# Performance work log

Hardware: AMD Instinct MI355X
Metric: run time of the kernel (lower is better)

## Reference

```python
import jax, jax.numpy as jnp
import numpy as np

NUM_HEADS = 8
LATENT_FRAME = 4
D_MODEL = 1024
D_FF = 1024  # dim_feedforward == output_dim in the torch module
N_LAYERS = 6
IN_DIM = 128
LN_EPS = 1e-5


def get_slopes(n):
    # standard ALiBi slopes for power-of-two head counts: 2^{-8(i+1)/n}
    return jnp.asarray([2.0 ** (-8.0 * (i + 1) / n) for i in range(n)], jnp.float32)


def alibi_mask(num_heads, T):
    # non-causal ('future') ALiBi: additive bias -slope_h * |i - j|, shape (H, T, T)
    dist = jnp.abs(jnp.arange(T)[:, None] - jnp.arange(T)[None, :]).astype(jnp.float32)
    return -get_slopes(num_heads)[:, None, None] * dist


def layernorm(x, g, b):
    m = jnp.mean(x, axis=-1, keepdims=True)
    v = jnp.mean((x - m) ** 2, axis=-1, keepdims=True)
    return (x - m) * jax.lax.rsqrt(v + LN_EPS) * g + b


def encoder_layer(x, p, mask):
    # torch TransformerEncoderLayer, post-norm, gelu(exact), dropout=0
    B, T, D = x.shape
    H, Dh = NUM_HEADS, D // NUM_HEADS
    qkv = x @ p['in_w'].T + p['in_b']                      # (B,T,3D)
    q, k, v = jnp.split(qkv, 3, axis=-1)
    hsplit = lambda t: t.reshape(B, T, H, Dh).transpose(0, 2, 1, 3)  # (B,H,T,Dh)
    q, k, v = hsplit(q), hsplit(k), hsplit(v)
    scores = jnp.einsum('bhqd,bhkd->bhqk', q, k) / float(np.sqrt(Dh)) + mask[None]
    attn = jax.nn.softmax(scores, axis=-1)
    o = jnp.einsum('bhqk,bhkd->bhqd', attn, v).transpose(0, 2, 1, 3).reshape(B, T, D)
    o = o @ p['out_w'].T + p['out_b']
    x = layernorm(x + o, p['ln1_g'], p['ln1_b'])
    ff = jax.nn.gelu(x @ p['ff1_w'].T + p['ff1_b'], approximate=False) @ p['ff2_w'].T + p['ff2_b']
    return layernorm(x + ff, p['ln2_g'], p['ln2_b'])


def setup_inputs() -> dict:
    key = jax.random.key(0)
    ks = iter(jax.random.split(key, 32))
    s = 0.02
    B, T, F = 8, 2048, IN_DIM
    Fs = F * LATENT_FRAME  # 512
    inp = {
        'x': jax.random.normal(next(ks), (B, T, F), jnp.float32),
        'pre_w': jax.random.normal(next(ks), (D_MODEL, Fs), jnp.float32) * s,
        'pre_b': jnp.zeros((D_MODEL,), jnp.float32),
        'in_w': jax.random.normal(next(ks), (N_LAYERS, 3 * D_MODEL, D_MODEL), jnp.float32) * s,
        'in_b': jnp.zeros((N_LAYERS, 3 * D_MODEL), jnp.float32),
        'out_w': jax.random.normal(next(ks), (N_LAYERS, D_MODEL, D_MODEL), jnp.float32) * s,
        'out_b': jnp.zeros((N_LAYERS, D_MODEL), jnp.float32),
        'ln1_g': jnp.ones((N_LAYERS, D_MODEL), jnp.float32),
        'ln1_b': jnp.zeros((N_LAYERS, D_MODEL), jnp.float32),
        'ff1_w': jax.random.normal(next(ks), (N_LAYERS, D_FF, D_MODEL), jnp.float32) * s,
        'ff1_b': jnp.zeros((N_LAYERS, D_FF), jnp.float32),
        'ff2_w': jax.random.normal(next(ks), (N_LAYERS, D_MODEL, D_FF), jnp.float32) * s,
        'ff2_b': jnp.zeros((N_LAYERS, D_MODEL), jnp.float32),
        'ln2_g': jnp.ones((N_LAYERS, D_MODEL), jnp.float32),
        'ln2_b': jnp.zeros((N_LAYERS, D_MODEL), jnp.float32),
        'post_w': jax.random.normal(next(ks), (D_MODEL, D_MODEL), jnp.float32) * s,
        'post_b': jnp.zeros((D_MODEL,), jnp.float32),
    }
    return inp


def reference(x, pre_w, pre_b, in_w, in_b, out_w, out_b, ln1_g, ln1_b,
              ff1_w, ff1_b, ff2_w, ff2_b, ln2_g, ln2_b, post_w, post_b):
    B, T, F = x.shape
    Tl = T // LATENT_FRAME
    x = x.reshape(B, Tl, F * LATENT_FRAME)
    x = x @ pre_w.T + pre_b                     # (B, Tl, D)
    mask = alibi_mask(NUM_HEADS, Tl)            # (H, Tl, Tl), shared by all batches
    layers = dict(in_w=in_w, in_b=in_b, out_w=out_w, out_b=out_b,
                  ln1_g=ln1_g, ln1_b=ln1_b, ff1_w=ff1_w, ff1_b=ff1_b,
                  ff2_w=ff2_w, ff2_b=ff2_b, ln2_g=ln2_g, ln2_b=ln2_b)
    def step(h, p):
        return encoder_layer(h, p, mask), None
    x, _ = jax.lax.scan(step, x, layers)
    return x @ post_w.T + post_b
```

## Files before the change

kernel.cpp:

```cpp
#include <hip/hip_runtime.h>
#include <hip/hip_bf16.h>

#define B 8
#define TL 512
#define M_ROWS 4096
#define D 1024
#define DFF 1024
#define H 8
#define DH 128
#define NL 6

typedef unsigned short ushort_t;
typedef unsigned int uint_t;
typedef short bf16x8 __attribute__((ext_vector_type(8)));
typedef float f32x4 __attribute__((ext_vector_type(4)));

__device__ __forceinline__ ushort_t f2bf(float f) {
    uint_t u = __float_as_uint(f);
    u += 0x7FFFu + ((u >> 16) & 1u);
    return (ushort_t)(u >> 16);
}
__device__ __forceinline__ float gelu_exact(float x) {
    return 0.5f * x * (1.0f + erff(x * 0.70710678118654752f));
}
__device__ __forceinline__ void gload_lds16(const ushort_t* g, ushort_t* l) {
    __builtin_amdgcn_global_load_lds(
        (const __attribute__((address_space(1))) void*)g,
        (__attribute__((address_space(3))) void*)l, 16, 0, 0);
}

struct CvtArgs {
    const float* s[7];
    ushort_t* d[7];
    int nq[7];
    int bstart[8];
};

__global__ __launch_bounds__(256) void cvt_all(CvtArgs a) {
    const int bid = blockIdx.x;
#pragma unroll
    for (int seg = 0; seg < 7; ++seg) {
        const int b0 = a.bstart[seg], b1 = a.bstart[seg + 1];
        if (bid < b0 || bid >= b1) continue;
        const int stride = (b1 - b0) * 256;
        const float* s = a.s[seg];
        ushort_t* d = a.d[seg];
        const int nq = a.nq[seg];
        for (int i = (bid - b0) * 256 + threadIdx.x; i < nq; i += stride) {
            float4 v = *(const float4*)(s + (size_t)i * 4);
            ushort4 o;
            o.x = f2bf(v.x); o.y = f2bf(v.y); o.z = f2bf(v.z); o.w = f2bf(v.w);
            *(ushort4*)(d + (size_t)i * 4) = o;
        }
    }
}

#define LSLOT64(r, c) (((r) * 8 + ((c) ^ ((r) & 7))) * 8)

#define PIPE_K_LOOP(NT)                                                        \
    {                                                                          \
        stage(0, 0);                                                           \
        stage(1, 64);                                                          \
        int bsel = 0;                                                          \
        for (int t = 0; t < (NT)-1; ++t) {                                     \
            asm volatile("s_waitcnt vmcnt(4)" ::: "memory");                   \
            __builtin_amdgcn_s_barrier();                                      \
            comp(bsel);                                                        \
            if (t + 2 < (NT)) {                                                \
                int nb = bsel + 2; if (nb >= 3) nb -= 3;                       \
                stage(nb, (t + 2) * 64);                                       \
            }                                                                  \
            ++bsel; if (bsel == 3) bsel = 0;                                   \
        }                                                                      \
        asm volatile("s_waitcnt vmcnt(0)" ::: "memory");                       \
        __builtin_amdgcn_s_barrier();                                          \
        comp(bsel);                                                            \
    }

__global__ __launch_bounds__(512) void gemm_n128(
    const ushort_t* __restrict__ A, const ushort_t* __restrict__ W,
    const float* __restrict__ bias, float* __restrict__ Cf,
    ushort_t* __restrict__ Cb, int M, int N, int K, int do_gelu) {
    extern __shared__ ushort_t lds[];

    const int tid = threadIdx.x;
    const int lane = tid & 63;
    const int w = tid >> 6;
    const int wm = w >> 2;
    const int wn = w & 3;
    const int bm = blockIdx.y * 128;
    const int bn = blockIdx.x * 128;
    const int fr = lane & 15;
    const int fq = lane >> 4;

    const ushort_t* gA[2];
    const ushort_t* gB[2];
    int sdst[2];
#pragma unroll
    for (int u = 0; u < 2; ++u) {
        int s = tid + u * 512;
        int r = s >> 3, c = (s & 7) ^ (r & 7);
        gA[u] = A + (size_t)(bm + r) * K + c * 8;
        gB[u] = W + (size_t)(bn + r) * K + c * 8;
        sdst[u] = s * 8;
    }

    int aoff[4][2], boff[2][2];
#pragma unroll
    for (int ti = 0; ti < 4; ++ti)
#pragma unroll
        for (int ks = 0; ks < 2; ++ks)
            aoff[ti][ks] = LSLOT64(wm * 64 + ti * 16 + fr, ks * 4 + fq);
#pragma unroll
    for (int tj = 0; tj < 2; ++tj)
#pragma unroll
        for (int ks = 0; ks < 2; ++ks)
            boff[tj][ks] = LSLOT64(wn * 32 + tj * 16 + fr, ks * 4 + fq);

    f32x4 acc[4][2];
#pragma unroll
    for (int i = 0; i < 4; ++i)
#pragma unroll
        for (int j = 0; j < 2; ++j) acc[i][j] = (f32x4){0.f, 0.f, 0.f, 0.f};

    auto stage = [&](int buf, int k0) {
#pragma unroll
        for (int u = 0; u < 2; ++u)
            gload_lds16(gA[u] + k0, &lds[buf * 16384 + sdst[u]]);
#pragma unroll
        for (int u = 0; u < 2; ++u)
            gload_lds16(gB[u] + k0, &lds[buf * 16384 + 8192 + sdst[u]]);
    };
    auto comp = [&](int buf) {
#pragma unroll
        for (int ks = 0; ks < 2; ++ks) {
            bf16x8 af[4], bfv[2];
#pragma unroll
            for (int ti = 0; ti < 4; ++ti)
                af[ti] = *(const bf16x8*)&lds[buf * 16384 + aoff[ti][ks]];
#pragma unroll
            for (int tj = 0; tj < 2; ++tj)
                bfv[tj] = *(const bf16x8*)&lds[buf * 16384 + 8192 + boff[tj][ks]];
            __builtin_amdgcn_s_setprio(1);
#pragma unroll
            for (int i = 0; i < 4; ++i)
#pragma unroll
                for (int j = 0; j < 2; ++j)
                    acc[i][j] = __builtin_amdgcn_mfma_f32_16x16x32_bf16(
                        af[i], bfv[j], acc[i][j], 0, 0, 0);
            __builtin_amdgcn_s_setprio(0);
        }
    };

    const int NT = K >> 6;
    PIPE_K_LOOP(NT)
    __syncthreads();

    float bv[2];
#pragma unroll
    for (int tj = 0; tj < 2; ++tj) bv[tj] = bias[bn + wn * 32 + tj * 16 + fr];

    float* eps = (float*)lds;
#pragma unroll
    for (int p = 0; p < 2; ++p) {
        if (p) __syncthreads();
        if (wm == p) {
#pragma unroll
            for (int ti = 0; ti < 4; ++ti)
#pragma unroll
                for (int tj = 0; tj < 2; ++tj)
#pragma unroll
                    for (int r = 0; r < 4; ++r) {
                        float v = acc[ti][tj][r] + bv[tj];
                        if (do_gelu) v = gelu_exact(v);
                        eps[(ti * 16 + fq * 4 + r) * 132 +
                            wn * 32 + tj * 16 + fr] = v;
                    }
        }
        __syncthreads();
#pragma unroll
        for (int k = 0; k < 4; ++k) {
            int f = tid + k * 512;
            int row = f >> 5, c4 = f & 31;
            float4 v = *(const float4*)&eps[row * 132 + c4 * 4];
            const size_t off = (size_t)(bm + p * 64 + row) * N + bn + c4 * 4;
            if (Cf) *(float4*)(Cf + off) = v;
            if (Cb) {
                ushort4 ob;
                ob.x = f2bf(v.x); ob.y = f2bf(v.y);
                ob.z = f2bf(v.z); ob.w = f2bf(v.w);
                *(ushort4*)(Cb + off) = ob;
            }
        }
    }
}

__global__ __launch_bounds__(512) void gemm_qkv128(
    const ushort_t* __restrict__ A, const ushort_t* __restrict__ W,
    const float* __restrict__ bias, ushort_t* __restrict__ Qb,
    ushort_t* __restrict__ Kb, ushort_t* __restrict__ Vt) {
    extern __shared__ ushort_t lds[];
    const int K = 1024;

    const int bid = blockIdx.x;
    const int wg = (bid & 7) * 96 + (bid >> 3);
    const int by = wg / 24, bx = wg - by * 24;
    const int bm = by * 128, bn = bx * 128;

    const int tid = threadIdx.x;
    const int lane = tid & 63;
    const int w = tid >> 6;
    const int wm = w >> 2;
    const int wn = w & 3;
    const int fr = lane & 15;
    const int fq = lane >> 4;

    const ushort_t* gA[2];
    const ushort_t* gB[2];
    int sdst[2];
#pragma unroll
    for (int u = 0; u < 2; ++u) {
        int s = tid + u * 512;
        int r = s >> 3, c = (s & 7) ^ (r & 7);
        gA[u] = A + (size_t)(bm + r) * K + c * 8;
        gB[u] = W + (size_t)(bn + r) * K + c * 8;
        sdst[u] = s * 8;
    }

    int aoff[4][2], boff[2][2];
#pragma unroll
    for (int ti = 0; ti < 4; ++ti)
#pragma unroll
        for (int ks = 0; ks < 2; ++ks)
            aoff[ti][ks] = LSLOT64(wm * 64 + ti * 16 + fr, ks * 4 + fq);
#pragma unroll
    for (int tj = 0; tj < 2; ++tj)
#pragma unroll
        for (int ks = 0; ks < 2; ++ks)
            boff[tj][ks] = LSLOT64(wn * 32 + tj * 16 + fr, ks * 4 + fq);

    f32x4 acc[4][2];
#pragma unroll
    for (int i = 0; i < 4; ++i)
#pragma unroll
        for (int j = 0; j < 2; ++j) acc[i][j] = (f32x4){0.f, 0.f, 0.f, 0.f};

    auto stage = [&](int buf, int k0) {
#pragma unroll
        for (int u = 0; u < 2; ++u)
            gload_lds16(gA[u] + k0, &lds[buf * 16384 + sdst[u]]);
#pragma unroll
        for (int u = 0; u < 2; ++u)
            gload_lds16(gB[u] + k0, &lds[buf * 16384 + 8192 + sdst[u]]);
    };
    auto comp = [&](int buf) {
#pragma unroll
        for (int ks = 0; ks < 2; ++ks) {
            bf16x8 af[4], bfv[2];
#pragma unroll
            for (int ti = 0; ti < 4; ++ti)
                af[ti] = *(const bf16x8*)&lds[buf * 16384 + aoff[ti][ks]];
#pragma unroll
            for (int tj = 0; tj < 2; ++tj)
                bfv[tj] = *(const bf16x8*)&lds[buf * 16384 + 8192 + boff[tj][ks]];
            __builtin_amdgcn_s_setprio(1);
#pragma unroll
            for (int i = 0; i < 4; ++i)
#pragma unroll
                for (int j = 0; j < 2; ++j)
                    acc[i][j] = __builtin_amdgcn_mfma_f32_16x16x32_bf16(
                        af[i], bfv[j], acc[i][j], 0, 0, 0);
            __builtin_amdgcn_s_setprio(0);
        }
    };

    PIPE_K_LOOP(16)

    const float qscale = 0.08838834764831845f;
    float bv[2];
#pragma unroll
    for (int tj = 0; tj < 2; ++tj) bv[tj] = bias[bn + wn * 32 + tj * 16 + fr];

    if (bn < 2 * D) {
        __syncthreads();
        const float scale = (bn < D) ? qscale : 1.f;
        ushort_t* dst = (bn < D) ? Qb : Kb;
        const int nc0 = (bn < D) ? bn : bn - D;
        float* eps = (float*)lds;
#pragma unroll
        for (int p = 0; p < 2; ++p) {
            if (p) __syncthreads();
            if (wm == p) {
#pragma unroll
                for (int ti = 0; ti < 4; ++ti)
#pragma unroll
                    for (int tj = 0; tj < 2; ++tj)
#pragma unroll
                        for (int r = 0; r < 4; ++r)
                            eps[(ti * 16 + fq * 4 + r) * 132 +
                                wn * 32 + tj * 16 + fr] =
                                (acc[ti][tj][r] + bv[tj]) * scale;
            }
            __syncthreads();
#pragma unroll
            for (int k = 0; k < 4; ++k) {
                int f = tid + k * 512;
                int row = f >> 5, c4 = f & 31;
                float4 v = *(const float4*)&eps[row * 132 + c4 * 4];
                ushort4 ob;
                ob.x = f2bf(v.x); ob.y = f2bf(v.y);
                ob.z = f2bf(v.z); ob.w = f2bf(v.w);
                *(ushort4*)(dst + (size_t)(bm + p * 64 + row) * D + nc0 +
                            c4 * 4) = ob;
            }
        }
    } else {
#pragma unroll
        for (int tj = 0; tj < 2; ++tj) {
            const int n = bn + wn * 32 + tj * 16 + fr;
            const int h = (n - 2 * D) >> 7;
            const int dh = (n - 2 * D) & 127;
#pragma unroll
            for (int ti = 0; ti < 4; ++ti) {
                const int m0 = bm + wm * 64 + ti * 16 + fq * 4;
                const int bb = m0 >> 9;
                const int t = m0 & 511;
                f32x4 a = acc[ti][tj];
                ushort4 pk;
                pk.x = f2bf(a[0] + bv[tj]); pk.y = f2bf(a[1] + bv[tj]);
                pk.z = f2bf(a[2] + bv[tj]); pk.w = f2bf(a[3] + bv[tj]);
                *(ushort4*)&Vt[((size_t)(bb * H + h) * DH + dh) * TL + t] = pk;
            }
        }
    }
}

#define LSW16(r, g) ((((r) << 4) + ((g) ^ ((r) & 7))) << 3)
#define LSW8(r, g) ((((r) << 3) + ((g) ^ ((r) & 7))) << 3)

__global__ __launch_bounds__(256, 2) void attn_mfma(
    const ushort_t* __restrict__ Qb, const ushort_t* __restrict__ Kb,
    const ushort_t* __restrict__ Vt, ushort_t* __restrict__ Ab) {
    __shared__ ushort_t Qs[64 * 128];
    __shared__ ushort_t Ks[64 * 128];
    __shared__ ushort_t Vts[128 * 64];
    __shared__ ushort_t Ps[64 * 72];

    const int q0 = blockIdx.x * 64;
    const int bh = blockIdx.y;
    const int b = bh >> 3;
    const int h = bh & 7;
    const int tid = threadIdx.x;
    const int lane = tid & 63;
    const int w = tid >> 6;
    const int fr = lane & 15;
    const int fq = lane >> 4;

    const float slope = exp2f(-(float)(h + 1));

#pragma unroll
    for (int kk = 0; kk < 4; ++kk) {
        int s = tid + kk * 256;
        int r = s >> 4, gp = s & 15, gl = gp ^ (r & 7);
        gload_lds16(Qb + (size_t)(b * TL + q0 + r) * D + h * DH + gl * 8,
                    &Qs[s * 8]);
    }

    f32x4 o8[8];
    float m_i[4], l_i[4];
#pragma unroll
    for (int nt = 0; nt < 8; ++nt) o8[nt] = (f32x4){0.f, 0.f, 0.f, 0.f};
#pragma unroll
    for (int r = 0; r < 4; ++r) { m_i[r] = -1e30f; l_i[r] = 0.f; }

    for (int kt = 0; kt < TL / 64; ++kt) {
        __syncthreads();
#pragma unroll
        for (int kk = 0; kk < 4; ++kk) {
            int s = tid + kk * 256;
            int r = s >> 4, gp = s & 15, gl = gp ^ (r & 7);
            gload_lds16(Kb + (size_t)(b * TL + kt * 64 + r) * D + h * DH + gl * 8,
                        &Ks[s * 8]);
        }
#pragma unroll
        for (int kk = 0; kk < 4; ++kk) {
            int s = tid + kk * 256;
            int r = s >> 3, gp = s & 7, gl = gp ^ (r & 7);
            gload_lds16(Vt + ((size_t)bh * DH + r) * TL + kt * 64 + gl * 8,
                        &Vts[s * 8]);
        }
        __syncthreads();

        f32x4 sacc[4];
#pragma unroll
        for (int jt = 0; jt < 4; ++jt) sacc[jt] = (f32x4){0.f, 0.f, 0.f, 0.f};
        __builtin_amdgcn_s_setprio(1);
#pragma unroll
        for (int s4 = 0; s4 < 4; ++s4) {
            bf16x8 aq = *(const bf16x8*)&Qs[LSW16(w * 16 + fr, s4 * 4 + fq)];
#pragma unroll
            for (int jt = 0; jt < 4; ++jt) {
                bf16x8 kb = *(const bf16x8*)&Ks[LSW16(jt * 16 + fr, s4 * 4 + fq)];
                sacc[jt] = __builtin_amdgcn_mfma_f32_16x16x32_bf16(
                    aq, kb, sacc[jt], 0, 0, 0);
            }
        }
        __builtin_amdgcn_s_setprio(0);

        const int iq = q0 + w * 16 + fq * 4;
        const int jk = kt * 64 + fr;
        float al[4];
#pragma unroll
        for (int r = 0; r < 4; ++r) {
            float sv[4];
#pragma unroll
            for (int jt = 0; jt < 4; ++jt)
                sv[jt] = sacc[jt][r] -
                         slope * fabsf((float)(iq + r - jk - jt * 16));
            float mx = fmaxf(fmaxf(sv[0], sv[1]), fmaxf(sv[2], sv[3]));
            mx = fmaxf(mx, __shfl_xor(mx, 1));
            mx = fmaxf(mx, __shfl_xor(mx, 2));
            mx = fmaxf(mx, __shfl_xor(mx, 4));
            mx = fmaxf(mx, __shfl_xor(mx, 8));
            float mnew = fmaxf(m_i[r], mx);
            al[r] = __expf(m_i[r] - mnew);
            float rs = 0.f;
#pragma unroll
            for (int jt = 0; jt < 4; ++jt) {
                sv[jt] = __expf(sv[jt] - mnew);
                rs += sv[jt];
            }
            rs += __shfl_xor(rs, 1);
            rs += __shfl_xor(rs, 2);
            rs += __shfl_xor(rs, 4);
            rs += __shfl_xor(rs, 8);
            l_i[r] = l_i[r] * al[r] + rs;
            m_i[r] = mnew;
            const int prow = w * 16 + fq * 4 + r;
#pragma unroll
            for (int jt = 0; jt < 4; ++jt)
                Ps[prow * 72 + jt * 16 + fr] = f2bf(sv[jt]);
        }
#pragma unroll
        for (int nt = 0; nt < 8; ++nt)
#pragma unroll
            for (int r = 0; r < 4; ++r) o8[nt][r] *= al[r];

        __builtin_amdgcn_s_setprio(1);
#pragma unroll
        for (int s2 = 0; s2 < 2; ++s2) {
            bf16x8 pa = *(const bf16x8*)&Ps[(w * 16 + fr) * 72 + s2 * 32 + fq * 8];
#pragma unroll
            for (int nt = 0; nt < 8; ++nt) {
                bf16x8 vb = *(const bf16x8*)&Vts[LSW8(nt * 16 + fr, s2 * 4 + fq)];
                o8[nt] = __builtin_amdgcn_mfma_f32_16x16x32_bf16(
                    pa, vb, o8[nt], 0, 0, 0);
            }
        }
        __builtin_amdgcn_s_setprio(0);
    }

#pragma unroll
    for (int r = 0; r < 4; ++r) {
        float inv = 1.f / l_i[r];
        const size_t base = (size_t)(b * TL + q0 + w * 16 + fq * 4 + r) * D + h * DH;
#pragma unroll
        for (int nt = 0; nt < 8; ++nt)
            Ab[base + nt * 16 + fr] = f2bf(o8[nt][r] * inv);
    }
}

__global__ __launch_bounds__(256) void add_ln(const float* __restrict__ x,
                                              const float* __restrict__ y,
                                              const float* __restrict__ g,
                                              const float* __restrict__ bta,
                                              float* __restrict__ out,
                                              ushort_t* __restrict__ outb) {
    const int row = blockIdx.x * 4 + (threadIdx.x >> 6);
    const int lane = threadIdx.x & 63;
    const size_t rbase = (size_t)row * D;

    float4 v[4];
#pragma unroll
    for (int j = 0; j < 4; ++j) {
        float4 xv = *(const float4*)(x + rbase + lane * 4 + j * 256);
        float4 yv = *(const float4*)(y + rbase + lane * 4 + j * 256);
        v[j].x = xv.x + yv.x; v[j].y = xv.y + yv.y;
        v[j].z = xv.z + yv.z; v[j].w = xv.w + yv.w;
    }

    float s = 0.f;
#pragma unroll
    for (int j = 0; j < 4; ++j) s += v[j].x + v[j].y + v[j].z + v[j].w;
#pragma unroll
    for (int off = 32; off; off >>= 1) s += __shfl_xor(s, off);
    const float mean = s * (1.f / (float)D);

    float sq = 0.f;
#pragma unroll
    for (int j = 0; j < 4; ++j) {
        float d0 = v[j].x - mean, d1 = v[j].y - mean;
        float d2 = v[j].z - mean, d3 = v[j].w - mean;
        sq += d0 * d0 + d1 * d1 + d2 * d2 + d3 * d3;
    }
#pragma unroll
    for (int off = 32; off; off >>= 1) sq += __shfl_xor(sq, off);
    const float var = sq * (1.f / (float)D);
    const float inv = rsqrtf(var + 1e-5f);

#pragma unroll
    for (int j = 0; j < 4; ++j) {
        const int col = lane * 4 + j * 256;
        float4 gv = *(const float4*)(g + col);
        float4 bv = *(const float4*)(bta + col);
        float4 o;
        o.x = (v[j].x - mean) * inv * gv.x + bv.x;
        o.y = (v[j].y - mean) * inv * gv.y + bv.y;
        o.z = (v[j].z - mean) * inv * gv.z + bv.z;
        o.w = (v[j].w - mean) * inv * gv.w + bv.w;
        *(float4*)(out + rbase + col) = o;
        ushort4 ob;
        ob.x = f2bf(o.x); ob.y = f2bf(o.y); ob.z = f2bf(o.z); ob.w = f2bf(o.w);
        *(ushort4*)(outb + rbase + col) = ob;
    }
}

extern "C" void kernel_launch(void* const* d_in, const int* in_sizes, int n_in,
                              void* d_out, int out_size, void* d_ws, size_t ws_size,
                              hipStream_t stream) {
    const float* x_in   = (const float*)d_in[0];
    const float* pre_w  = (const float*)d_in[1];
    const float* pre_b  = (const float*)d_in[2];
    const float* in_w   = (const float*)d_in[3];
    const float* in_b   = (const float*)d_in[4];
    const float* out_w  = (const float*)d_in[5];
    const float* out_b  = (const float*)d_in[6];
    const float* ln1_g  = (const float*)d_in[7];
    const float* ln1_b  = (const float*)d_in[8];
    const float* ff1_w  = (const float*)d_in[9];
    const float* ff1_b  = (const float*)d_in[10];
    const float* ff2_w  = (const float*)d_in[11];
    const float* ff2_b  = (const float*)d_in[12];
    const float* ln2_g  = (const float*)d_in[13];
    const float* ln2_b  = (const float*)d_in[14];
    const float* post_w = (const float*)d_in[15];
    const float* post_b = (const float*)d_in[16];

    static bool attr_set = false;
    if (!attr_set) {
        hipFuncSetAttribute((const void*)gemm_n128,
                            hipFuncAttributeMaxDynamicSharedMemorySize, 98304);
        hipFuncSetAttribute((const void*)gemm_qkv128,
                            hipFuncAttributeMaxDynamicSharedMemorySize, 98304);
        attr_set = true;
    }

    float* X = (float*)d_ws;
    float* Y = X + (size_t)M_ROWS * D;
    ushort_t* Xb   = (ushort_t*)(Y + (size_t)M_ROWS * D);
    ushort_t* Ab   = Xb + (size_t)M_ROWS * D;
    ushort_t* Qb   = Ab + (size_t)M_ROWS * D;
    ushort_t* Kb   = Qb + (size_t)M_ROWS * D;
    ushort_t* Vt   = Kb + (size_t)M_ROWS * D;
    ushort_t* xinb = Vt + (size_t)M_ROWS * D;
    ushort_t* pwb  = xinb + (size_t)M_ROWS * 512;
    ushort_t* iwb  = pwb + (size_t)D * 512;
    ushort_t* owb  = iwb + (size_t)NL * 3 * D * D;
    ushort_t* f1wb = owb + (size_t)NL * D * D;
    ushort_t* f2wb = f1wb + (size_t)NL * DFF * D;
    ushort_t* powb = f2wb + (size_t)NL * D * DFF;

    const dim3 blk(256);

    CvtArgs ca;
    ca.s[0] = x_in;   ca.d[0] = xinb; ca.nq[0] = (M_ROWS * 512) / 4;
    ca.s[1] = pre_w;  ca.d[1] = pwb;  ca.nq[1] = (D * 512) / 4;
    ca.s[2] = in_w;   ca.d[2] = iwb;  ca.nq[2] = (NL * 3 * D * D) / 4;
    ca.s[3] = out_w;  ca.d[3] = owb;  ca.nq[3] = (NL * D * D) / 4;
    ca.s[4] = ff1_w;  ca.d[4] = f1wb; ca.nq[4] = (NL * DFF * D) / 4;
    ca.s[5] = ff2_w;  ca.d[5] = f2wb; ca.nq[5] = (NL * D * DFF) / 4;
    ca.s[6] = post_w; ca.d[6] = powb; ca.nq[6] = (D * D) / 4;
    {
        long long total = 0;
        for (int i = 0; i < 7; ++i) total += ca.nq[i];
        long long cum = 0;
        ca.bstart[0] = 0;
        for (int i = 0; i < 7; ++i) {
            cum += ca.nq[i];
            ca.bstart[i + 1] = (int)((cum * 4096) / total);
        }
        ca.bstart[7] = 4096;
    }
    cvt_all<<<4096, blk, 0, stream>>>(ca);

    const dim3 gN128(D / 128, M_ROWS / 128);

    gemm_n128<<<gN128, dim3(512), 98304, stream>>>(xinb, pwb, pre_b, X, Xb,
                                                   M_ROWS, D, 512, 0);

    for (int l = 0; l < NL; ++l) {
        gemm_qkv128<<<dim3(768), dim3(512), 98304, stream>>>(
            Xb, iwb + (size_t)l * 3 * D * D, in_b + (size_t)l * 3 * D,
            Qb, Kb, Vt);
        attn_mfma<<<dim3(TL / 64, B * H), blk, 0, stream>>>(Qb, Kb, Vt, Ab);
        gemm_n128<<<gN128, dim3(512), 98304, stream>>>(
            Ab, owb + (size_t)l * D * D, out_b + (size_t)l * D, Y, nullptr,
            M_ROWS, D, D, 0);
        add_ln<<<dim3(M_ROWS / 4), blk, 0, stream>>>(X, Y, ln1_g + (size_t)l * D,
                                                     ln1_b + (size_t)l * D, X, Xb);
        gemm_n128<<<gN128, dim3(512), 98304, stream>>>(
            Xb, f1wb + (size_t)l * DFF * D, ff1_b + (size_t)l * DFF, nullptr, Ab,
            M_ROWS, DFF, D, 1);
        gemm_n128<<<gN128, dim3(512), 98304, stream>>>(
            Ab, f2wb + (size_t)l * D * DFF, ff2_b + (size_t)l * D, Y, nullptr,
            M_ROWS, D, DFF, 0);
        add_ln<<<dim3(M_ROWS / 4), blk, 0, stream>>>(X, Y, ln2_g + (size_t)l * D,
                                                     ln2_b + (size_t)l * D, X, Xb);
    }

    gemm_n128<<<gN128, dim3(512), 98304, stream>>>(Xb, powb, post_b,
                                                   (float*)d_out, nullptr,
                                                   M_ROWS, D, D, 0);
}
```

Before: 1.082 ms.

## Double-buffer GEMM LDS, prefetch K/V in attention, nontemporal weight conversion

The GEMM kernels change from a triple-buffered LDS pipeline to a double-buffered one with an extra barrier per k-step. This cuts dynamic LDS from 96KB to 64KB, which may allow more blocks per CU. The attention kernel holds Q in registers and double-buffers K and V tiles with explicit vmcnt waits, so loads overlap compute instead of being synchronous each iteration. The bf16 conversion kernel uses nontemporal loads and stores. The risk is less latency hiding in the GEMMs and more barrier overhead.

```diff
diff --git a/kernel.cpp b/kernel.cpp
--- a/kernel.cpp
+++ b/kernel.cpp
@@ -12,6 +12,7 @@
 
 typedef unsigned short ushort_t;
 typedef unsigned int uint_t;
+typedef unsigned long long u64_t;
 typedef short bf16x8 __attribute__((ext_vector_type(8)));
 typedef float f32x4 __attribute__((ext_vector_type(4)));
 
@@ -47,34 +48,34 @@
         ushort_t* d = a.d[seg];
         const int nq = a.nq[seg];
         for (int i = (bid - b0) * 256 + threadIdx.x; i < nq; i += stride) {
-            float4 v = *(const float4*)(s + (size_t)i * 4);
-            ushort4 o;
-            o.x = f2bf(v.x); o.y = f2bf(v.y); o.z = f2bf(v.z); o.w = f2bf(v.w);
-            *(ushort4*)(d + (size_t)i * 4) = o;
+            f32x4 v = __builtin_nontemporal_load(
+                (const f32x4*)(s + (size_t)i * 4));
+            u64_t pk = (u64_t)f2bf(v[0]) | ((u64_t)f2bf(v[1]) << 16) |
+                       ((u64_t)f2bf(v[2]) << 32) | ((u64_t)f2bf(v[3]) << 48);
+            __builtin_nontemporal_store(pk, (u64_t*)(d + (size_t)i * 4));
         }
     }
 }
 
 #define LSLOT64(r, c) (((r) * 8 + ((c) ^ ((r) & 7))) * 8)
 
-#define PIPE_K_LOOP(NT)                                                        \
+#define PIPE2_K_LOOP(NT)                                                       \
     {                                                                          \
         stage(0, 0);                                                           \
         stage(1, 64);                                                          \
-        int bsel = 0;                                                          \
         for (int t = 0; t < (NT)-1; ++t) {                                     \
             asm volatile("s_waitcnt vmcnt(4)" ::: "memory");                   \
             __builtin_amdgcn_s_barrier();                                      \
-            comp(bsel);                                                        \
-            if (t + 2 < (NT)) {                                                \
-                int nb = bsel + 2; if (nb >= 3) nb -= 3;                       \
-                stage(nb, (t + 2) * 64);                                       \
-            }                                                                  \
-            ++bsel; if (bsel == 3) bsel = 0;                                   \
+            asm volatile("" ::: "memory");                                     \
+            comp(t & 1);                                                       \
+            __builtin_amdgcn_s_barrier();                                      \
+            asm volatile("" ::: "memory");                                     \
+            if (t + 2 < (NT)) stage(t & 1, (t + 2) * 64);                      \
         }                                                                      \
         asm volatile("s_waitcnt vmcnt(0)" ::: "memory");                       \
         __builtin_amdgcn_s_barrier();                                          \
-        comp(bsel);                                                            \
+        asm volatile("" ::: "memory");                                         \
+        comp(((NT)-1) & 1);                                                    \
     }
 
 __global__ __launch_bounds__(512) void gemm_n128(
@@ -153,7 +154,7 @@
     };
 
     const int NT = K >> 6;
-    PIPE_K_LOOP(NT)
+    PIPE2_K_LOOP(NT)
     __syncthreads();
 
     float bv[2];
@@ -274,7 +275,7 @@
         }
     };
 
-    PIPE_K_LOOP(16)
+    PIPE2_K_LOOP(16)
 
     const float qscale = 0.08838834764831845f;
     float bv[2];
@@ -341,9 +342,8 @@
 __global__ __launch_bounds__(256, 2) void attn_mfma(
     const ushort_t* __restrict__ Qb, const ushort_t* __restrict__ Kb,
     const ushort_t* __restrict__ Vt, ushort_t* __restrict__ Ab) {
-    __shared__ ushort_t Qs[64 * 128];
-    __shared__ ushort_t Ks[64 * 128];
-    __shared__ ushort_t Vts[128 * 64];
+    __shared__ ushort_t Ks[2][64 * 128];
+    __shared__ ushort_t Vts[2][128 * 64];
     __shared__ ushort_t Ps[64 * 72];
 
     const int q0 = blockIdx.x * 64;
@@ -358,13 +358,46 @@
 
     const float slope = exp2f(-(float)(h + 1));
 
+    auto stageK = [&](int buf, int kt) {
+#pragma unroll
+        for (int kk = 0; kk < 4; ++kk) {
+            int s = tid + kk * 256;
+            int r = s >> 4, gl = (s & 15) ^ (r & 7);
+            gload_lds16(Kb + (size_t)(b * TL + kt * 64 + r) * D + h * DH + gl * 8,
+                        &Ks[buf][s * 8]);
+        }
+    };
+    auto stageV = [&](int buf, int kt) {
+#pragma unroll
+        for (int kk = 0; kk < 4; ++kk) {
+            int s = tid + kk * 256;
+            int r = s >> 3, gl = (s & 7) ^ (r & 7);
+            gload_lds16(Vt + ((size_t)bh * DH + r) * TL + kt * 64 + gl * 8,
+                        &Vts[buf][s * 8]);
+        }
+    };
+
 #pragma unroll
     for (int kk = 0; kk < 4; ++kk) {
         int s = tid + kk * 256;
-        int r = s >> 4, gp = s & 15, gl = gp ^ (r & 7);
+        int r = s >> 4, gl = (s & 15) ^ (r & 7);
         gload_lds16(Qb + (size_t)(b * TL + q0 + r) * D + h * DH + gl * 8,
-                    &Qs[s * 8]);
-    }
+                    &Ks[0][s * 8]);
+    }
+    asm volatile("s_waitcnt vmcnt(0)" ::: "memory");
+    __builtin_amdgcn_s_barrier();
+    asm volatile("" ::: "memory");
+    bf16x8 aq[4];
+#pragma unroll
+    for (int s4 = 0; s4 < 4; ++s4)
+        aq[s4] = *(const bf16x8*)&Ks[0][LSW16(w * 16 + fr, s4 * 4 + fq)];
+    asm volatile("s_waitcnt lgkmcnt(0)" ::: "memory");
+    __builtin_amdgcn_s_barrier();
+    asm volatile("" ::: "memory");
+
+    stageK(0, 0);
+    stageV(0, 0);
+    stageK(1, 1);
 
     f32x4 o8[8];
     float m_i[4], l_i[4];
@@ -373,23 +406,12 @@
 #pragma unroll
     for (int r = 0; r < 4; ++r) { m_i[r] = -1e30f; l_i[r] = 0.f; }
 
+#pragma unroll 1
     for (int kt = 0; kt < TL / 64; ++kt) {
-        __syncthreads();
-#pragma unroll
-        for (int kk = 0; kk < 4; ++kk) {
-            int s = tid + kk * 256;
-            int r = s >> 4, gp = s & 15, gl = gp ^ (r & 7);
-            gload_lds16(Kb + (size_t)(b * TL + kt * 64 + r) * D + h * DH + gl * 8,
-                        &Ks[s * 8]);
-        }
-#pragma unroll
-        for (int kk = 0; kk < 4; ++kk) {
-            int s = tid + kk * 256;
-            int r = s >> 3, gp = s & 7, gl = gp ^ (r & 7);
-            gload_lds16(Vt + ((size_t)bh * DH + r) * TL + kt * 64 + gl * 8,
-                        &Vts[s * 8]);
-        }
-        __syncthreads();
+        const int kb = kt & 1;
+        asm volatile("s_waitcnt vmcnt(8)" ::: "memory");
+        __builtin_amdgcn_s_barrier();
+        asm volatile("" ::: "memory");
 
         f32x4 sacc[4];
 #pragma unroll
@@ -397,12 +419,11 @@
         __builtin_amdgcn_s_setprio(1);
 #pragma unroll
         for (int s4 = 0; s4 < 4; ++s4) {
-            bf16x8 aq = *(const bf16x8*)&Qs[LSW16(w * 16 + fr, s4 * 4 + fq)];
 #pragma unroll
             for (int jt = 0; jt < 4; ++jt) {
-                bf16x8 kb = *(const bf16x8*)&Ks[LSW16(jt * 16 + fr, s4 * 4 + fq)];
+                bf16x8 kbv = *(const bf16x8*)&Ks[kb][LSW16(jt * 16 + fr, s4 * 4 + fq)];
                 sacc[jt] = __builtin_amdgcn_mfma_f32_16x16x32_bf16(
-                    aq, kb, sacc[jt], 0, 0, 0);
+                    aq[s4], kbv, sacc[jt], 0, 0, 0);
             }
         }
         __builtin_amdgcn_s_setprio(0);
@@ -446,13 +467,30 @@
 #pragma unroll
             for (int r = 0; r < 4; ++r) o8[nt][r] *= al[r];
 
+        asm volatile("s_waitcnt lgkmcnt(0)" ::: "memory");
+        __builtin_amdgcn_s_barrier();
+        asm volatile("" ::: "memory");
+
+        if (kt + 2 < TL / 64) stageK(kb, kt + 2);
+        if (kt + 1 < TL / 64) stageV(kb ^ 1, kt + 1);
+
+        if (kt < 6) {
+            asm volatile("s_waitcnt vmcnt(8)" ::: "memory");
+        } else if (kt == 6) {
+            asm volatile("s_waitcnt vmcnt(4)" ::: "memory");
+        } else {
+            asm volatile("s_waitcnt vmcnt(0)" ::: "memory");
+        }
+        __builtin_amdgcn_s_barrier();
+        asm volatile("" ::: "memory");
+
         __builtin_amdgcn_s_setprio(1);
 #pragma unroll
         for (int s2 = 0; s2 < 2; ++s2) {
             bf16x8 pa = *(const bf16x8*)&Ps[(w * 16 + fr) * 72 + s2 * 32 + fq * 8];
 #pragma unroll
             for (int nt = 0; nt < 8; ++nt) {
-                bf16x8 vb = *(const bf16x8*)&Vts[LSW8(nt * 16 + fr, s2 * 4 + fq)];
+                bf16x8 vb = *(const bf16x8*)&Vts[kb][LSW8(nt * 16 + fr, s2 * 4 + fq)];
                 o8[nt] = __builtin_amdgcn_mfma_f32_16x16x32_bf16(
                     pa, vb, o8[nt], 0, 0, 0);
             }
@@ -549,9 +587,9 @@
     static bool attr_set = false;
     if (!attr_set) {
         hipFuncSetAttribute((const void*)gemm_n128,
-                            hipFuncAttributeMaxDynamicSharedMemorySize, 98304);
+                            hipFuncAttributeMaxDynamicSharedMemorySize, 65536);
         hipFuncSetAttribute((const void*)gemm_qkv128,
-                            hipFuncAttributeMaxDynamicSharedMemorySize, 98304);
+                            hipFuncAttributeMaxDynamicSharedMemorySize, 65536);
         attr_set = true;
     }
 
@@ -595,30 +633,30 @@
 
     const dim3 gN128(D / 128, M_ROWS / 128);
 
-    gemm_n128<<<gN128, dim3(512), 98304, stream>>>(xinb, pwb, pre_b, X, Xb,
+    gemm_n128<<<gN128, dim3(512), 65536, stream>>>(xinb, pwb, pre_b, X, Xb,
                                                    M_ROWS, D, 512, 0);
 
     for (int l = 0; l < NL; ++l) {
-        gemm_qkv128<<<dim3(768), dim3(512), 98304, stream>>>(
+        gemm_qkv128<<<dim3(768), dim3(512), 65536, stream>>>(
             Xb, iwb + (size_t)l * 3 * D * D, in_b + (size_t)l * 3 * D,
             Qb, Kb, Vt);
         attn_mfma<<<dim3(TL / 64, B * H), blk, 0, stream>>>(Qb, Kb, Vt, Ab);
-        gemm_n128<<<gN128, dim3(512), 98304, stream>>>(
+        gemm_n128<<<gN128, dim3(512), 65536, stream>>>(
             Ab, owb + (size_t)l * D * D, out_b + (size_t)l * D, Y, nullptr,
             M_ROWS, D, D, 0);
         add_ln<<<dim3(M_ROWS / 4), blk, 0, stream>>>(X, Y, ln1_g + (size_t)l * D,
                                                      ln1_b + (size_t)l * D, X, Xb);
-        gemm_n128<<<gN128, dim3(512), 98304, stream>>>(
+        gemm_n128<<<gN128, dim3(512), 65536, stream>>>(
             Xb, f1wb + (size_t)l * DFF * D, ff1_b + (size_t)l * DFF, nullptr, Ab,
             M_ROWS, DFF, D, 1);
-        gemm_n128<<<gN128, dim3(512), 98304, stream>>>(
+        gemm_n128<<<gN128, dim3(512), 65536, stream>>>(
             Ab, f2wb + (size_t)l * D * DFF, ff2_b + (size_t)l * D, Y, nullptr,
             M_ROWS, D, DFF, 0);
         add_ln<<<dim3(M_ROWS / 4), blk, 0, stream>>>(X, Y, ln2_g + (size_t)l * D,
                                                      ln2_b + (size_t)l * D, X, Xb);
     }
 
-    gemm_n128<<<gN128, dim3(512), 98304, stream>>>(Xb, powb, post_b,
+    gemm_n128<<<gN128, dim3(512), 65536, stream>>>(Xb, powb, post_b,
                                                    (float*)d_out, nullptr,
                                                    M_ROWS, D, D, 0);
 }
```

Result: slower. 1.108 ms (+2.4%).
